# Optimization experiments

Measured on AMD Instinct MI355X. Metric: run time of the kernel, lower is better.

Reference implementation:

```python
import jax, jax.numpy as jnp
import numpy as np

B, S = 32, 512
POS, EMBED, HIDDEN, NHEAD, FF, NBLOCKS = 2, 128, 128, 4, 512, 2
C_CLIP = 10.0
NEG = -1e9
HD = EMBED // NHEAD      # mha head dim
GHD = HIDDEN // NHEAD    # glimpse head dim


def setup_inputs() -> dict:
    keys = iter(jax.random.split(jax.random.key(0), 64))
    def nrm(shape, s=0.05):
        return jax.random.normal(next(keys), shape, dtype=jnp.float32) * s
    def zeros(shape):
        return jnp.zeros(shape, jnp.float32)
    inp = {}
    inp["inputs"] = jax.random.uniform(next(keys), (B, S, POS), dtype=jnp.float32)
    inp["emb_w"] = nrm((EMBED, POS)); inp["emb_b"] = zeros((EMBED,))
    inp["in_proj_w"] = nrm((NBLOCKS, 3 * EMBED, EMBED)); inp["in_proj_b"] = zeros((NBLOCKS, 3 * EMBED))
    inp["out_proj_w"] = nrm((NBLOCKS, EMBED, EMBED)); inp["out_proj_b"] = zeros((NBLOCKS, EMBED))
    inp["ff1_w"] = nrm((NBLOCKS, FF, EMBED)); inp["ff1_b"] = zeros((NBLOCKS, FF))
    inp["ff2_w"] = nrm((NBLOCKS, EMBED, FF)); inp["ff2_b"] = zeros((NBLOCKS, EMBED))
    inp["hctx_w"] = nrm((EMBED, EMBED)); inp["hctx_b"] = zeros((EMBED,))
    inp["vw_w"] = nrm((EMBED, POS * EMBED)); inp["vw_b"] = zeros((EMBED,))
    inp["init_w"] = jax.random.uniform(next(keys), (POS * EMBED,), dtype=jnp.float32, minval=-1.0, maxval=1.0)
    inp["gq_w"] = nrm((HIDDEN, EMBED)); inp["gq_b"] = zeros((HIDDEN,))
    inp["gk_w"] = nrm((HIDDEN, EMBED)); inp["gk_b"] = zeros((HIDDEN,))
    inp["gv_w"] = nrm((HIDDEN, EMBED)); inp["gv_b"] = zeros((HIDDEN,))
    inp["go_w"] = nrm((EMBED, HIDDEN)); inp["go_b"] = zeros((EMBED,))
    inp["pq_w"] = nrm((HIDDEN, EMBED)); inp["pq_b"] = zeros((HIDDEN,))
    inp["pk_w"] = nrm((HIDDEN, EMBED)); inp["pk_b"] = zeros((HIDDEN,))
    return inp


def _mha(x, wi, bi, wo, bo):
    # torch.nn.MultiheadAttention self-attention, batch-first layout here
    b, s, e = x.shape
    qkv = x @ wi.T + bi                       # [B,S,3E]
    q, k, v = jnp.split(qkv, 3, axis=-1)
    q = q.reshape(b, s, NHEAD, HD) * (HD ** -0.5)
    k = k.reshape(b, s, NHEAD, HD)
    v = v.reshape(b, s, NHEAD, HD)
    attn = jax.nn.softmax(jnp.einsum('bqhd,bkhd->bhqk', q, k), axis=-1)
    o = jnp.einsum('bhqk,bkhd->bqhd', attn, v).reshape(b, s, e)
    return o @ wo.T + bo


def _encode(inputs, emb_w, emb_b, in_proj_w, in_proj_b, out_proj_w, out_proj_b,
            ff1_w, ff1_b, ff2_w, ff2_b):
    h = inputs @ emb_w.T + emb_b              # LinearEmbedding: [B,S,E]
    for l in range(NBLOCKS):
        h = h + _mha(h, in_proj_w[l], in_proj_b[l], out_proj_w[l], out_proj_b[l])
        h = h + (jax.nn.relu(h @ ff1_w[l].T + ff1_b[l]) @ ff2_w[l].T + ff2_b[l])
    return h


def _forward(inputs, emb_w, emb_b, in_proj_w, in_proj_b, out_proj_w, out_proj_b,
             ff1_w, ff1_b, ff2_w, ff2_b, hctx_w, hctx_b, vw_w, vw_b, init_w,
             gq_w, gq_b, gk_w, gk_b, gv_w, gv_b, go_w, go_b, pq_w, pq_b, pk_w, pk_b):
    h = _encode(inputs, emb_w, emb_b, in_proj_w, in_proj_b, out_proj_w, out_proj_b,
                ff1_w, ff1_b, ff2_w, ff2_b)           # [B,S,E]
    h_bar = h.mean(axis=1) @ hctx_w.T + hctx_b         # [B,E]
    query0 = h_bar + (init_w @ vw_w.T + vw_b)          # [B,E] (broadcast)
    query0 = jnp.broadcast_to(query0, (B, EMBED))
    # keys/values of glimpse and pointer depend only on h: precompute once
    gk = (h @ gk_w.T + gk_b).reshape(B, S, NHEAD, GHD)
    gv = (h @ gv_w.T + gv_b).reshape(B, S, NHEAD, GHD)
    pk = h @ pk_w.T + pk_b                             # [B,S,H]
    skey = jax.random.key(42)
    batch_idx = jnp.arange(B)

    def step(carry, t):
        mask, query, first_h = carry
        # masked multi-head glimpse attention
        gq = (query @ gq_w.T + gq_b).reshape(B, NHEAD, GHD)
        gl = jnp.einsum('bhd,bshd->bhs', gq, gk) * (GHD ** -0.5)
        gl = jnp.where(mask[:, None, :], NEG, gl)
        alpha = jax.nn.softmax(gl, axis=-1)
        n_query = jnp.einsum('bhs,bshd->bhd', alpha, gv).reshape(B, HIDDEN) @ go_w.T + go_b
        # tanh-clipped pointer attention
        pq = n_query @ pq_w.T + pq_b
        pl = C_CLIP * jnp.tanh(jnp.einsum('bd,bsd->bs', pq, pk) * (HIDDEN ** -0.5))
        pl = jnp.where(mask, NEG, pl)
        logp = jax.nn.log_softmax(pl, axis=-1)
        chosen = jax.random.categorical(jax.random.fold_in(skey, t), pl)   # [B]
        logprob = logp[batch_idx, chosen]
        mask = mask.at[batch_idx, chosen].set(True)
        chosen_h = h[batch_idx, chosen]                # gather chosen embedding
        first_h = jnp.where(t == 0, chosen_h, first_h)
        h_rest = jnp.concatenate([first_h, chosen_h], axis=-1) @ vw_w.T + vw_b
        return (mask, h_bar + h_rest, first_h), (logprob, chosen)

    init = (jnp.zeros((B, S), dtype=bool), query0, jnp.zeros((B, EMBED), jnp.float32))
    _, (logprobs, indices) = jax.lax.scan(step, init, jnp.arange(S))
    return logprobs.T, indices.T                       # [B,S], [B,S]


def reference(inputs, emb_w, emb_b, in_proj_w, in_proj_b, out_proj_w, out_proj_b,
              ff1_w, ff1_b, ff2_w, ff2_b, hctx_w, hctx_b, vw_w, vw_b, init_w,
              gq_w, gq_b, gk_w, gk_b, gv_w, gv_b, go_w, go_b, pq_w, pq_b, pk_w, pk_b):
    return _forward(inputs, emb_w, emb_b, in_proj_w, in_proj_b, out_proj_w, out_proj_b,
                    ff1_w, ff1_b, ff2_w, ff2_b, hctx_w, hctx_b, vw_w, vw_b, init_w,
                    gq_w, gq_b, gk_w, gk_b, gv_w, gv_b, go_w, go_b, pq_w, pq_b, pk_w, pk_b)
```

## Files before the change

kernel.cpp:

```cpp
#include <hip/hip_runtime.h>
#include <hip/hip_bf16.h>
#include <cstdint>

#define NEGV  (-1e9f)

__device__ __forceinline__ void threefry2x32(uint32_t k0, uint32_t k1,
                                             uint32_t x0, uint32_t x1,
                                             uint32_t& o0, uint32_t& o1) {
  uint32_t ks0 = k0, ks1 = k1, ks2 = k0 ^ k1 ^ 0x1BD11BDAu;
  x0 += ks0; x1 += ks1;
#define TF_RND(r) { x0 += x1; x1 = (x1 << (r)) | (x1 >> (32 - (r))); x1 ^= x0; }
  TF_RND(13) TF_RND(15) TF_RND(26) TF_RND(6)
  x0 += ks1; x1 += ks2 + 1u;
  TF_RND(17) TF_RND(29) TF_RND(16) TF_RND(24)
  x0 += ks2; x1 += ks0 + 2u;
  TF_RND(13) TF_RND(15) TF_RND(26) TF_RND(6)
  x0 += ks0; x1 += ks1 + 3u;
  TF_RND(17) TF_RND(29) TF_RND(16) TF_RND(24)
  x0 += ks1; x1 += ks2 + 4u;
  TF_RND(13) TF_RND(15) TF_RND(26) TF_RND(6)
  x0 += ks2; x1 += ks0 + 5u;
#undef TF_RND
  o0 = x0; o1 = x1;
}

__global__ __launch_bounds__(256) void gumbel_kernel(float* __restrict__ gt) {
  int idx = blockIdx.x * 256 + threadIdx.x;
  int t = idx >> 14, i = idx & 16383;
  uint32_t k0, k1;
  threefry2x32(0u, 42u, 0u, (uint32_t)t, k0, k1);
  uint32_t o0, o1;
  threefry2x32(k0, k1, 0u, (uint32_t)i, o0, o1);
  uint32_t bits = o0 ^ o1;
  uint32_t fb = (bits >> 9) | 0x3f800000u;
  float f = __uint_as_float(fb) - 1.0f;
  float u = (f == 0.f) ? 1.17549435e-38f : f;
  gt[idx] = (float)(-log(-log((double)u)));
}

__global__ __launch_bounds__(256) void embed_kernel(const float* __restrict__ in,
    const float* __restrict__ w, const float* __restrict__ b, float* __restrict__ h) {
  int idx = blockIdx.x * 256 + threadIdx.x;
  int t = idx >> 7, e = idx & 127;
  h[idx] = in[t * 2] * w[e * 2] + in[t * 2 + 1] * w[e * 2 + 1] + b[e];
}

template<int OP>
__global__ __launch_bounds__(256) void gemm_kernel(const float* __restrict__ A,
    const float* __restrict__ W, const float* __restrict__ bias,
    const float* __restrict__ R, float* __restrict__ out, int N, int K) {
  __shared__ float As[64][36];
  __shared__ float Bs[64][36];
  int tid = threadIdx.x;
  int tx = tid & 15, ty = tid >> 4;
  int row0 = blockIdx.y * 64, col0 = blockIdx.x * 64;
  const int sa = (ty & 7) << 2, sb = (tx & 7) << 2;
  float acc[4][4] = {};
  for (int k0 = 0; k0 < K; k0 += 32) {
#pragma unroll
    for (int l = 0; l < 2; l++) {
      int idx = tid + l * 256;
      int r = idx >> 3, c = (idx & 7) * 4;
      int cs = c ^ (((r >> 2) & 7) << 2);
      *(float4*)&As[r][cs] = *(const float4*)&A[(size_t)(row0 + r) * K + k0 + c];
      *(float4*)&Bs[r][cs] = *(const float4*)&W[(size_t)(col0 + r) * K + k0 + c];
    }
    __syncthreads();
#pragma unroll
    for (int kq = 0; kq < 32; kq += 4) {
      float4 a4[4], b4[4];
#pragma unroll
      for (int u = 0; u < 4; u++) {
        a4[u] = *(const float4*)&As[ty * 4 + u][kq ^ sa];
        b4[u] = *(const float4*)&Bs[tx * 4 + u][kq ^ sb];
      }
      float aq[4][4], bq[4][4];
#pragma unroll
      for (int u = 0; u < 4; u++) {
        aq[u][0] = a4[u].x; aq[u][1] = a4[u].y; aq[u][2] = a4[u].z; aq[u][3] = a4[u].w;
        bq[u][0] = b4[u].x; bq[u][1] = b4[u].y; bq[u][2] = b4[u].z; bq[u][3] = b4[u].w;
      }
#pragma unroll
      for (int q = 0; q < 4; q++)
#pragma unroll
        for (int i = 0; i < 4; i++)
#pragma unroll
          for (int j = 0; j < 4; j++)
            acc[i][j] += aq[i][q] * bq[j][q];
    }
    __syncthreads();
  }
#pragma unroll
  for (int i = 0; i < 4; i++) {
    int r = row0 + ty * 4 + i;
#pragma unroll
    for (int j = 0; j < 4; j++) {
      int c = col0 + tx * 4 + j;
      float v = acc[i][j] + bias[c];
      if (OP == 1) v = fmaxf(v, 0.f);
      if (OP == 2) v += R[(size_t)r * N + c];
      if (OP == 3)      out[(((size_t)(c >> 2)) * 16384 + r) * 4 + (c & 3)] = v;
      else if (OP == 4) out[(((size_t)(r >> 2)) * N + c) * 4 + (r & 3)] = v;
      else              out[(size_t)r * N + c] = v;
    }
  }
}

__global__ __launch_bounds__(256) void wtr4_kernel(const float* __restrict__ in,
    float* __restrict__ out, int J, int K) {
  int idx = blockIdx.x * 256 + threadIdx.x;
  if (idx >= J * K) return;
  int j = idx / K, k = idx % K;
  out[((size_t)(k >> 2) * J + j) * 4 + (k & 3)] = in[(size_t)j * K + k];
}

__global__ __launch_bounds__(256) void wsplit_kernel(const float* __restrict__ in,
    float* __restrict__ outL, float* __restrict__ outR) {
  int idx = blockIdx.x * 256 + threadIdx.x;
  if (idx >= 16384) return;
  int j = idx >> 7, k = idx & 127;
  outL[idx] = in[(size_t)j * 256 + k];
  outR[idx] = in[(size_t)j * 256 + 128 + k];
}

#define ATTN_LDS_FLOATS (2*512*33 + 128 + 4*513 + 512)
__global__ __launch_bounds__(256) void attn_kernel(const float* __restrict__ qkv,
                                                   float* __restrict__ aout) {
  extern __shared__ float sm[];
  float* Ks = sm;
  float* Vs = Ks + 512 * 33;
  float* qs = Vs + 512 * 33;
  float* P  = qs + 128;
  float* red = P + 4 * 513;
  int tid = threadIdx.x;
  int lane = tid & 63, wv = tid >> 6;
  int b = blockIdx.x >> 2, h = blockIdx.x & 3;
  const float scale = 0.17677669529663687f;
  const size_t base = (size_t)b * 512 * 384;
  for (int idx = tid; idx < 512 * 32; idx += 256) {
    int s = idx >> 5, d = idx & 31;
    Ks[s * 33 + d] = qkv[base + (size_t)s * 384 + 128 + h * 32 + d];
    Vs[s * 33 + d] = qkv[base + (size_t)s * 384 + 256 + h * 32 + d];
  }
  __syncthreads();
  for (int q0 = 0; q0 < 512; q0 += 4) {
    if (tid < 128) {
      int r = tid >> 5, d = tid & 31;
      qs[r * 32 + d] = qkv[base + (size_t)(q0 + r) * 384 + h * 32 + d] * scale;
    }
    __syncthreads();
    for (int s = tid; s < 512; s += 256) {
      float a0 = 0, a1 = 0, a2 = 0, a3 = 0;
      const float* kr = Ks + s * 33;
#pragma unroll 8
      for (int d = 0; d < 32; d++) {
        float kv = kr[d];
        a0 += qs[d] * kv; a1 += qs[32 + d] * kv; a2 += qs[64 + d] * kv; a3 += qs[96 + d] * kv;
      }
      P[0 * 513 + s] = a0; P[1 * 513 + s] = a1; P[2 * 513 + s] = a2; P[3 * 513 + s] = a3;
    }
    __syncthreads();
    float v0[4], v1[4], mx[4], sums[4];
#pragma unroll
    for (int r = 0; r < 4; r++) { v0[r] = P[r * 513 + tid]; v1[r] = P[r * 513 + tid + 256]; }
#pragma unroll
    for (int r = 0; r < 4; r++) {
      float x = fmaxf(v0[r], v1[r]);
      for (int off = 32; off; off >>= 1) x = fmaxf(x, __shfl_xor(x, off));
      if (lane == 0) red[wv * 4 + r] = x;
    }
    __syncthreads();
#pragma unroll
    for (int r = 0; r < 4; r++) {
      float x = red[r];
      for (int w = 1; w < 4; w++) x = fmaxf(x, red[w * 4 + r]);
      mx[r] = x;
    }
    __syncthreads();
#pragma unroll
    for (int r = 0; r < 4; r++) {
      float e0 = expf(v0[r] - mx[r]), e1 = expf(v1[r] - mx[r]);
      P[r * 513 + tid] = e0; P[r * 513 + tid + 256] = e1;
      float x = e0 + e1;
      for (int off = 32; off; off >>= 1) x += __shfl_xor(x, off);
      if (lane == 0) red[wv * 4 + r] = x;
    }
    __syncthreads();
#pragma unroll
    for (int r = 0; r < 4; r++) {
      float x = 0;
      for (int w = 0; w < 4; w++) x += red[w * 4 + r];
      sums[r] = x;
    }
#pragma unroll
    for (int r = 0; r < 4; r++) {
      P[r * 513 + tid] /= sums[r];
      P[r * 513 + tid + 256] /= sums[r];
    }
    __syncthreads();
    {
      int d = tid & 31, p = tid >> 5;
      float a0 = 0, a1 = 0, a2 = 0, a3 = 0;
#pragma unroll 4
      for (int i = 0; i < 64; i++) {
        int s = p * 64 + i;
        float vv = Vs[s * 33 + d];
        a0 += P[0 * 513 + s] * vv; a1 += P[1 * 513 + s] * vv;
        a2 += P[2 * 513 + s] * vv; a3 += P[3 * 513 + s] * vv;
      }
      a0 += __shfl_xor(a0, 32); a1 += __shfl_xor(a1, 32);
      a2 += __shfl_xor(a2, 32); a3 += __shfl_xor(a3, 32);
      if (lane < 32) {
        red[wv * 128 + 0 * 32 + d] = a0;
        red[wv * 128 + 1 * 32 + d] = a1;
        red[wv * 128 + 2 * 32 + d] = a2;
        red[wv * 128 + 3 * 32 + d] = a3;
      }
    }
    __syncthreads();
    if (tid < 128) {
      int r = tid >> 5, d = tid & 31;
      float x = red[0 * 128 + r * 32 + d] + red[1 * 128 + r * 32 + d]
              + red[2 * 128 + r * 32 + d] + red[3 * 128 + r * 32 + d];
      aout[(size_t)(b * 512 + q0 + r) * 128 + h * 32 + d] = x;
    }
    __syncthreads();
  }
}

__global__ __launch_bounds__(128) void hbar_kernel(const float* __restrict__ h,
    const float* __restrict__ hctx_w, const float* __restrict__ hctx_b,
    float* __restrict__ h_bar) {
  __shared__ float m[128];
  int b = blockIdx.x, e = threadIdx.x;
  float s = 0.f;
  for (int t = 0; t < 512; t++) s += h[((size_t)b * 512 + t) * 128 + e];
  m[e] = s * (1.0f / 512.0f);
  __syncthreads();
  float acc = hctx_b[e];
  for (int k = 0; k < 128; k++) acc += m[k] * hctx_w[e * 128 + k];
  h_bar[b * 128 + e] = acc;
}

__global__ __launch_bounds__(128) void vproj_kernel(const float* __restrict__ init_w,
    const float* __restrict__ vw_w, const float* __restrict__ vw_b,
    float* __restrict__ vproj) {
  int j = threadIdx.x;
  float acc = vw_b[j];
  for (int k = 0; k < 256; k++) acc += init_w[k] * vw_w[j * 256 + k];
  vproj[j] = acc;
}

__global__ __launch_bounds__(512) void decode_kernel(
    const float* __restrict__ gv4, const float* __restrict__ gkT4,
    const float* __restrict__ pkT4, const float* __restrict__ h_bar,
    const float* __restrict__ vproj,
    const float* __restrict__ gq_wT, const float* __restrict__ gq_b,
    const float* __restrict__ go_wT, const float* __restrict__ go_b,
    const float* __restrict__ pq_wT, const float* __restrict__ pq_b,
    const float* __restrict__ vw_b, const float* __restrict__ gt,
    const float* __restrict__ P2L, const float* __restrict__ P2R,
    float* __restrict__ out) {
  int b = blockIdx.x;
  int tid = threadIdx.x;
  int lane = tid & 63, wave = tid >> 6;
  int j = tid & 127, p = tid >> 7;
  __shared__ float query[128], hbar_s[128], gqv[128], nq[128], nq2[128], pqv[128];
  __shared__ float part[512];
  __shared__ float gl[4 * 512];
  __shared__ float pl[512];
  __shared__ int   mask[512];
  __shared__ float redf[32], redf2[32];
  __shared__ float redv[8]; __shared__ int redi[8];
  __shared__ float redm2[8], reds2[8];

  const float4* gv4b = (const float4*)gv4 + (size_t)b * 16384;
  const float4* gk4  = (const float4*)gkT4 + (size_t)b * 512;
  const float4* pk4  = (const float4*)pkT4 + (size_t)b * 512;
  const float*  gtb  = gt + (size_t)b * 512;
  const float*  p2lB = P2L + (size_t)b * 65536;
  const float*  p2rB = P2R + (size_t)b * 65536;

  if (tid < 128) {
    float hbv = h_bar[b * 128 + tid];
    hbar_s[tid] = hbv;
    query[tid] = hbv + vproj[tid];
  }
  mask[tid] = 0;
  int fc = 0;
  __syncthreads();

  for (int t = 0; t < 512; t++) {
    float gum = gtb[(size_t)t * 16384 + tid];

    {
      const float4* q4 = (const float4*)query + p * 8;
      const float4* w4 = (const float4*)gq_wT + (size_t)(p * 8) * 128 + j;
      float acc = 0.f;
#pragma unroll
      for (int i = 0; i < 8; i++) {
        float4 x4 = q4[i]; float4 ww = w4[(size_t)i * 128];
        acc += x4.x * ww.x; acc += x4.y * ww.y; acc += x4.z * ww.z; acc += x4.w * ww.w;
      }
      part[p * 128 + j] = acc;
    }
    __syncthreads();
    if (tid < 128)
      gqv[tid] = (part[tid] + part[128 + tid]) + (part[256 + tid] + part[384 + tid]) + gq_b[tid];
    __syncthreads();

    float v[4];
    {
      bool msk = (mask[tid] != 0);
      const float4* q4 = (const float4*)gqv;
#pragma unroll
      for (int hh = 0; hh < 4; hh++) {
        float acc = 0.f;
#pragma unroll
        for (int i = 0; i < 8; i++) {
          float4 qq = q4[hh * 8 + i];
          float4 gg = gk4[(size_t)(hh * 8 + i) * 16384 + tid];
          acc += qq.x * gg.x; acc += qq.y * gg.y; acc += qq.z * gg.z; acc += qq.w * gg.w;
        }
        v[hh] = msk ? NEGV : acc * 0.17677669529663687f;
      }
#pragma unroll
      for (int hh = 0; hh < 4; hh++) {
        float x = v[hh];
        for (int off = 32; off; off >>= 1) x = fmaxf(x, __shfl_xor(x, off));
        if (lane == 0) redf[wave * 4 + hh] = x;
      }
    }
    __syncthreads();
    float e[4];
    {
#pragma unroll
      for (int hh = 0; hh < 4; hh++) {
        float x = redf[hh];
        for (int w = 1; w < 8; w++) x = fmaxf(x, redf[w * 4 + hh]);
        e[hh] = expf(v[hh] - x);
        float sx = e[hh];
        for (int off = 32; off; off >>= 1) sx += __shfl_xor(sx, off);
        if (lane == 0) redf2[wave * 4 + hh] = sx;
      }
    }
    __syncthreads();
    {
#pragma unroll
      for (int hh = 0; hh < 4; hh++) {
        float x = 0.f;
        for (int w = 0; w < 8; w++) x += redf2[w * 4 + hh];
        gl[hh * 512 + tid] = e[hh] / x;
      }
    }
    __syncthreads();

    {
      int hh = j >> 5;
      const float4* al4 = (const float4*)(gl + hh * 512 + p * 128);
      const float4* gp  = gv4b + (size_t)(p * 32) * 128 + j;
      float acc = 0.f;
#pragma unroll 8
      for (int i = 0; i < 32; i++) {
        float4 aa = al4[i]; float4 vv = gp[(size_t)i * 128];
        acc += aa.x * vv.x; acc += aa.y * vv.y; acc += aa.z * vv.z; acc += aa.w * vv.w;
      }
      part[p * 128 + j] = acc;
    }
    __syncthreads();
    if (tid < 128)
      nq[tid] = (part[tid] + part[128 + tid]) + (part[256 + tid] + part[384 + tid]);
    __syncthreads();

    {
      const float4* q4 = (const float4*)nq + p * 8;
      const float4* w4 = (const float4*)go_wT + (size_t)(p * 8) * 128 + j;
      float acc = 0.f;
#pragma unroll
      for (int i = 0; i < 8; i++) {
        float4 x4 = q4[i]; float4 ww = w4[(size_t)i * 128];
        acc += x4.x * ww.x; acc += x4.y * ww.y; acc += x4.z * ww.z; acc += x4.w * ww.w;
      }
      part[p * 128 + j] = acc;
    }
    __syncthreads();
    if (tid < 128)
      nq2[tid] = (part[tid] + part[128 + tid]) + (part[256 + tid] + part[384 + tid]) + go_b[tid];
    __syncthreads();

    {
      const float4* q4 = (const float4*)nq2 + p * 8;
      const float4* w4 = (const float4*)pq_wT + (size_t)(p * 8) * 128 + j;
      float acc = 0.f;
#pragma unroll
      for (int i = 0; i < 8; i++) {
        float4 x4 = q4[i]; float4 ww = w4[(size_t)i * 128];
        acc += x4.x * ww.x; acc += x4.y * ww.y; acc += x4.z * ww.z; acc += x4.w * ww.w;
      }
      part[p * 128 + j] = acc;
    }
    __syncthreads();
    if (tid < 128)
      pqv[tid] = (part[tid] + part[128 + tid]) + (part[256 + tid] + part[384 + tid]) + pq_b[tid];
    __syncthreads();

    {
      const float4* q4 = (const float4*)pqv;
      float acc = 0.f;
#pragma unroll 8
      for (int i = 0; i < 32; i++) {
        float4 qq = q4[i];
        float4 pp = pk4[(size_t)i * 16384 + tid];
        acc += qq.x * pp.x; acc += qq.y * pp.y; acc += qq.z * pp.z; acc += qq.w * pp.w;
      }
      float vv = 10.0f * tanhf(acc * 0.08838834764831843f);
      float plv = (mask[tid] != 0) ? NEGV : vv;
      pl[tid] = plv;
      float pgv = plv + gum;
      float av = pgv; int ix = tid;
      float mp = plv;
      for (int off = 32; off; off >>= 1) {
        float ov = __shfl_xor(av, off); int oi = __shfl_xor(ix, off);
        if (ov > av || (ov == av && oi < ix)) { av = ov; ix = oi; }
        mp = fmaxf(mp, __shfl_xor(mp, off));
      }
      float ee = expf(plv - mp);
      for (int off = 32; off; off >>= 1) ee += __shfl_xor(ee, off);
      if (lane == 0) { redv[wave] = av; redi[wave] = ix; redm2[wave] = mp; reds2[wave] = ee; }
    }
    __syncthreads();

    int c;
    {
      float av = redv[0]; c = redi[0];
#pragma unroll
      for (int w = 1; w < 8; w++) {
        if (redv[w] > av || (redv[w] == av && redi[w] < c)) { av = redv[w]; c = redi[w]; }
      }
      if (t == 0) fc = c;
      if (tid == 0) {
        float M = redm2[0];
        for (int w = 1; w < 8; w++) M = fmaxf(M, redm2[w]);
        float S = 0.f;
        for (int w = 0; w < 8; w++) S += reds2[w] * expf(redm2[w] - M);
        out[b * 512 + t] = pl[c] - M - logf(S);
        out[16384 + b * 512 + t] = (float)c;
        mask[c] = 1;
      }
    }
    __syncthreads();

    if (tid < 128) {
      float p2 = p2lB[(size_t)fc * 128 + tid] + p2rB[(size_t)c * 128 + tid];
      query[tid] = hbar_s[tid] + (p2 + vw_b[tid]);
    }
    __syncthreads();
  }
}

extern "C" void kernel_launch(void* const* d_in, const int* in_sizes, int n_in,
                              void* d_out, int out_size, void* d_ws, size_t ws_size,
                              hipStream_t stream) {
  (void)in_sizes; (void)n_in; (void)out_size; (void)ws_size;
  const float* inputs     = (const float*)d_in[0];
  const float* emb_w      = (const float*)d_in[1];
  const float* emb_b      = (const float*)d_in[2];
  const float* in_proj_w  = (const float*)d_in[3];
  const float* in_proj_b  = (const float*)d_in[4];
  const float* out_proj_w = (const float*)d_in[5];
  const float* out_proj_b = (const float*)d_in[6];
  const float* ff1_w      = (const float*)d_in[7];
  const float* ff1_b      = (const float*)d_in[8];
  const float* ff2_w      = (const float*)d_in[9];
  const float* ff2_b      = (const float*)d_in[10];
  const float* hctx_w     = (const float*)d_in[11];
  const float* hctx_b     = (const float*)d_in[12];
  const float* vw_w       = (const float*)d_in[13];
  const float* vw_b       = (const float*)d_in[14];
  const float* init_w     = (const float*)d_in[15];
  const float* gq_w = (const float*)d_in[16]; const float* gq_b = (const float*)d_in[17];
  const float* gk_w = (const float*)d_in[18]; const float* gk_b = (const float*)d_in[19];
  const float* gv_w = (const float*)d_in[20]; const float* gv_b = (const float*)d_in[21];
  const float* go_w = (const float*)d_in[22]; const float* go_b = (const float*)d_in[23];
  const float* pq_w = (const float*)d_in[24]; const float* pq_b = (const float*)d_in[25];
  const float* pk_w = (const float*)d_in[26]; const float* pk_b = (const float*)d_in[27];
  float* out = (float*)d_out;

  float* ws   = (float*)d_ws;
  float* h    = ws;
  float* s1   = h + 2097152;
  float* s2   = s1 + 8388608;
  float* hbar = s2 + 2097152;
  float* vpj  = hbar + 4096;
  float* wqT  = vpj + 128;
  float* woT  = wqT + 16384;
  float* wpT  = woT + 16384;
  float* vwL  = wpT + 16384;
  float* vwR  = vwL + 16384;
  float* zeros= vwR + 16384;
  float* gtab = zeros + 128;
  float* P2Lb = s1;
  float* gv4  = s1 + 2097152;
  float* pkT4 = s1 + 4194304;
  float* P2Rb = s1 + 6291456;
  float* gkT4 = s2;

  const int attn_lds = ATTN_LDS_FLOATS * 4;
  hipFuncSetAttribute((const void*)attn_kernel,
                      hipFuncAttributeMaxDynamicSharedMemorySize, attn_lds);

  gumbel_kernel<<<32768, 256, 0, stream>>>(gtab);
  embed_kernel<<<8192, 256, 0, stream>>>(inputs, emb_w, emb_b, h);
  for (int l = 0; l < 2; l++) {
    gemm_kernel<0><<<dim3(6, 256), 256, 0, stream>>>(
        h, in_proj_w + (size_t)l * 384 * 128, in_proj_b + l * 384, nullptr, s1, 384, 128);
    attn_kernel<<<128, 256, attn_lds, stream>>>(s1, s2);
    gemm_kernel<2><<<dim3(2, 256), 256, 0, stream>>>(
        s2, out_proj_w + (size_t)l * 128 * 128, out_proj_b + l * 128, h, h, 128, 128);
    gemm_kernel<1><<<dim3(8, 256), 256, 0, stream>>>(
        h, ff1_w + (size_t)l * 512 * 128, ff1_b + l * 512, nullptr, s1, 512, 128);
    gemm_kernel<2><<<dim3(2, 256), 256, 0, stream>>>(
        s1, ff2_w + (size_t)l * 128 * 512, ff2_b + l * 128, h, h, 128, 512);
  }
  hipMemsetAsync(zeros, 0, 512, stream);
  gemm_kernel<3><<<dim3(2, 256), 256, 0, stream>>>(h, gk_w, gk_b, nullptr, gkT4, 128, 128);
  gemm_kernel<4><<<dim3(2, 256), 256, 0, stream>>>(h, gv_w, gv_b, nullptr, gv4, 128, 128);
  gemm_kernel<3><<<dim3(2, 256), 256, 0, stream>>>(h, pk_w, pk_b, nullptr, pkT4, 128, 128);
  wtr4_kernel<<<64, 256, 0, stream>>>(gq_w, wqT, 128, 128);
  wtr4_kernel<<<64, 256, 0, stream>>>(go_w, woT, 128, 128);
  wtr4_kernel<<<64, 256, 0, stream>>>(pq_w, wpT, 128, 128);
  wsplit_kernel<<<64, 256, 0, stream>>>(vw_w, vwL, vwR);
  gemm_kernel<0><<<dim3(2, 256), 256, 0, stream>>>(h, vwL, zeros, nullptr, P2Lb, 128, 128);
  gemm_kernel<0><<<dim3(2, 256), 256, 0, stream>>>(h, vwR, zeros, nullptr, P2Rb, 128, 128);
  hbar_kernel<<<32, 128, 0, stream>>>(h, hctx_w, hctx_b, hbar);
  vproj_kernel<<<1, 128, 0, stream>>>(init_w, vw_w, vw_b, vpj);
  decode_kernel<<<32, 512, 0, stream>>>(gv4, gkT4, pkT4, hbar, vpj,
      wqT, gq_b, woT, go_b, wpT, pq_b, vw_b, gtab, P2Lb, P2Rb, out);
}
```

Baseline: 12.90 ms.

## Double decode block to 1024 threads, splitting head and key-dot work across halves

The sequential decode kernel now launches 1024 threads per batch instead of 512. The glimpse score/softmax (split by head pairs), the attention-value reduction and the pointer-key dot product (split along the hidden dim) are divided between the two halves, with extra shared buffers to combine partials. The aim is to cut per-step latency in this 32-block, latency-bound loop by spreading the memory-heavy dot products over more waves. In exchange it adds one extra barrier per step, leaves the upper half idle during the small matvecs, and puts more register pressure on each thread.

```diff
diff --git a/kernel.cpp b/kernel.cpp
--- a/kernel.cpp
+++ b/kernel.cpp
@@ -251,7 +251,7 @@
   vproj[j] = acc;
 }
 
-__global__ __launch_bounds__(512) void decode_kernel(
+__global__ __launch_bounds__(1024) void decode_kernel(
     const float* __restrict__ gv4, const float* __restrict__ gkT4,
     const float* __restrict__ pkT4, const float* __restrict__ h_bar,
     const float* __restrict__ vproj,
@@ -263,16 +263,19 @@
     float* __restrict__ out) {
   int b = blockIdx.x;
   int tid = threadIdx.x;
+  bool lo = (tid < 512);
+  int s = tid & 511;
   int lane = tid & 63, wave = tid >> 6;
-  int j = tid & 127, p = tid >> 7;
+  int j = tid & 127, p = (tid >> 7) & 3;
+  int half = tid >> 9;
   __shared__ float query[128], hbar_s[128], gqv[128], nq[128], nq2[128], pqv[128];
-  __shared__ float part[512];
+  __shared__ float part[512], part2[512];
   __shared__ float gl[4 * 512];
-  __shared__ float pl[512];
+  __shared__ float pl[512], plh[512];
   __shared__ int   mask[512];
   __shared__ float redf[32], redf2[32];
-  __shared__ float redv[8]; __shared__ int redi[8];
-  __shared__ float redm2[8], reds2[8];
+  __shared__ float redv[16]; __shared__ int redi[16];
+  __shared__ float redm2[16], reds2[16];
 
   const float4* gv4b = (const float4*)gv4 + (size_t)b * 16384;
   const float4* gk4  = (const float4*)gkT4 + (size_t)b * 512;
@@ -286,14 +289,15 @@
     hbar_s[tid] = hbv;
     query[tid] = hbv + vproj[tid];
   }
-  mask[tid] = 0;
+  if (lo) mask[tid] = 0;
   int fc = 0;
   __syncthreads();
 
   for (int t = 0; t < 512; t++) {
-    float gum = gtb[(size_t)t * 16384 + tid];
-
-    {
+    float gum = 0.f;
+    if (lo) gum = gtb[(size_t)t * 16384 + tid];
+
+    if (lo) {
       const float4* q4 = (const float4*)query + p * 8;
       const float4* w4 = (const float4*)gq_wT + (size_t)(p * 8) * 128 + j;
       float acc = 0.f;
@@ -309,70 +313,80 @@
       gqv[tid] = (part[tid] + part[128 + tid]) + (part[256 + tid] + part[384 + tid]) + gq_b[tid];
     __syncthreads();
 
-    float v[4];
-    {
-      bool msk = (mask[tid] != 0);
+    float v[2];
+    {
+      bool msk = (mask[s] != 0);
       const float4* q4 = (const float4*)gqv;
-#pragma unroll
-      for (int hh = 0; hh < 4; hh++) {
+      int hb = half * 2;
+#pragma unroll
+      for (int lh = 0; lh < 2; lh++) {
+        int hh = hb + lh;
         float acc = 0.f;
 #pragma unroll
         for (int i = 0; i < 8; i++) {
           float4 qq = q4[hh * 8 + i];
-          float4 gg = gk4[(size_t)(hh * 8 + i) * 16384 + tid];
+          float4 gg = gk4[(size_t)(hh * 8 + i) * 16384 + s];
           acc += qq.x * gg.x; acc += qq.y * gg.y; acc += qq.z * gg.z; acc += qq.w * gg.w;
         }
-        v[hh] = msk ? NEGV : acc * 0.17677669529663687f;
-      }
-#pragma unroll
-      for (int hh = 0; hh < 4; hh++) {
-        float x = v[hh];
+        v[lh] = msk ? NEGV : acc * 0.17677669529663687f;
+      }
+#pragma unroll
+      for (int lh = 0; lh < 2; lh++) {
+        float x = v[lh];
         for (int off = 32; off; off >>= 1) x = fmaxf(x, __shfl_xor(x, off));
-        if (lane == 0) redf[wave * 4 + hh] = x;
-      }
-    }
-    __syncthreads();
-    float e[4];
-    {
-#pragma unroll
-      for (int hh = 0; hh < 4; hh++) {
-        float x = redf[hh];
-        for (int w = 1; w < 8; w++) x = fmaxf(x, redf[w * 4 + hh]);
-        e[hh] = expf(v[hh] - x);
-        float sx = e[hh];
+        if (lane == 0) redf[wave * 2 + lh] = x;
+      }
+    }
+    __syncthreads();
+    float e[2];
+    {
+      int wb = half * 8;
+#pragma unroll
+      for (int lh = 0; lh < 2; lh++) {
+        float x = redf[wb * 2 + lh];
+        for (int w = 1; w < 8; w++) x = fmaxf(x, redf[(wb + w) * 2 + lh]);
+        e[lh] = expf(v[lh] - x);
+        float sx = e[lh];
         for (int off = 32; off; off >>= 1) sx += __shfl_xor(sx, off);
-        if (lane == 0) redf2[wave * 4 + hh] = sx;
-      }
-    }
-    __syncthreads();
-    {
-#pragma unroll
-      for (int hh = 0; hh < 4; hh++) {
+        if (lane == 0) redf2[wave * 2 + lh] = sx;
+      }
+    }
+    __syncthreads();
+    {
+      int wb = half * 8, hb = half * 2;
+#pragma unroll
+      for (int lh = 0; lh < 2; lh++) {
         float x = 0.f;
-        for (int w = 0; w < 8; w++) x += redf2[w * 4 + hh];
-        gl[hh * 512 + tid] = e[hh] / x;
+        for (int w = 0; w < 8; w++) x += redf2[(wb + w) * 2 + lh];
+        gl[(hb + lh) * 512 + s] = e[lh] / x;
       }
     }
     __syncthreads();
 
     {
       int hh = j >> 5;
-      const float4* al4 = (const float4*)(gl + hh * 512 + p * 128);
-      const float4* gp  = gv4b + (size_t)(p * 32) * 128 + j;
+      const float4* al4 = (const float4*)(gl + hh * 512 + p * 128) + half * 16;
+      const float4* gp  = gv4b + (size_t)((p * 32 + half * 16)) * 128 + j;
       float acc = 0.f;
-#pragma unroll 8
-      for (int i = 0; i < 32; i++) {
+#pragma unroll
+      for (int i = 0; i < 16; i++) {
         float4 aa = al4[i]; float4 vv = gp[(size_t)i * 128];
         acc += aa.x * vv.x; acc += aa.y * vv.y; acc += aa.z * vv.z; acc += aa.w * vv.w;
       }
-      part[p * 128 + j] = acc;
-    }
-    __syncthreads();
-    if (tid < 128)
-      nq[tid] = (part[tid] + part[128 + tid]) + (part[256 + tid] + part[384 + tid]);
-    __syncthreads();
-
-    {
+      if (half) part2[p * 128 + j] = acc;
+      else      part[p * 128 + j] = acc;
+    }
+    __syncthreads();
+    if (tid < 128) {
+      float p0 = part[tid] + part2[tid];
+      float p1 = part[128 + tid] + part2[128 + tid];
+      float p2 = part[256 + tid] + part2[256 + tid];
+      float p3 = part[384 + tid] + part2[384 + tid];
+      nq[tid] = (p0 + p1) + (p2 + p3);
+    }
+    __syncthreads();
+
+    if (lo) {
       const float4* q4 = (const float4*)nq + p * 8;
       const float4* w4 = (const float4*)go_wT + (size_t)(p * 8) * 128 + j;
       float acc = 0.f;
@@ -388,7 +402,7 @@
       nq2[tid] = (part[tid] + part[128 + tid]) + (part[256 + tid] + part[384 + tid]) + go_b[tid];
     __syncthreads();
 
-    {
+    if (lo) {
       const float4* q4 = (const float4*)nq2 + p * 8;
       const float4* w4 = (const float4*)pq_wT + (size_t)(p * 8) * 128 + j;
       float acc = 0.f;
@@ -404,20 +418,27 @@
       pqv[tid] = (part[tid] + part[128 + tid]) + (part[256 + tid] + part[384 + tid]) + pq_b[tid];
     __syncthreads();
 
+    float accL;
     {
       const float4* q4 = (const float4*)pqv;
+      const int ib = half * 16;
       float acc = 0.f;
-#pragma unroll 8
-      for (int i = 0; i < 32; i++) {
-        float4 qq = q4[i];
-        float4 pp = pk4[(size_t)i * 16384 + tid];
+#pragma unroll
+      for (int i = 0; i < 16; i++) {
+        float4 qq = q4[ib + i];
+        float4 pp = pk4[(size_t)(ib + i) * 16384 + s];
         acc += qq.x * pp.x; acc += qq.y * pp.y; acc += qq.z * pp.z; acc += qq.w * pp.w;
       }
+      if (lo) accL = acc; else plh[s] = acc;
+    }
+    __syncthreads();
+    if (lo) {
+      float acc = accL + plh[s];
       float vv = 10.0f * tanhf(acc * 0.08838834764831843f);
-      float plv = (mask[tid] != 0) ? NEGV : vv;
-      pl[tid] = plv;
+      float plv = (mask[s] != 0) ? NEGV : vv;
+      pl[s] = plv;
       float pgv = plv + gum;
-      float av = pgv; int ix = tid;
+      float av = pgv; int ix = s;
       float mp = plv;
       for (int off = 32; off; off >>= 1) {
         float ov = __shfl_xor(av, off); int oi = __shfl_xor(ix, off);
@@ -534,6 +555,6 @@
   gemm_kernel<0><<<dim3(2, 256), 256, 0, stream>>>(h, vwR, zeros, nullptr, P2Rb, 128, 128);
   hbar_kernel<<<32, 128, 0, stream>>>(h, hctx_w, hctx_b, hbar);
   vproj_kernel<<<1, 128, 0, stream>>>(init_w, vw_w, vw_b, vpj);
-  decode_kernel<<<32, 512, 0, stream>>>(gv4, gkT4, pkT4, hbar, vpj,
+  decode_kernel<<<32, 1024, 0, stream>>>(gv4, gkT4, pkT4, hbar, vpj,
       wqT, gq_b, woT, go_b, wpT, pq_b, vw_b, gtab, P2Lb, P2Rb, out);
 }
```

Result: slower. 15.37 ms (+19.1%).
